# Kernel tuning notes

Hardware: AMD Instinct MI355X
Metric: run time of the kernel (lower is better)

Reference implementation:

```python
import jax, jax.numpy as jnp
import numpy as np

X_SCALE, X_ZP = 0.03, -66.0
Y_SCALE, Y_ZP = 0.025, 160.0  # per-tensor quant params for uint8 y


def setup_inputs() -> dict:
    key = jax.random.key(0)
    kx, ky = jax.random.split(key)
    # x simulates int8 values in [-128, 127], stored as fp32
    x = jax.random.randint(kx, (7, 8, 1024, 1024), 0, 256).astype(jnp.float32) - 128.0
    # y simulates uint8 values in [0, 255], stored as fp32
    y = jax.random.randint(ky, (8, 1024, 1024), 0, 256).astype(jnp.float32)
    return {"x": x, "y": y}


def reference(x, y):
    # dequantize: (q - zero_point) * scale
    qx = (x - X_ZP) * X_SCALE              # [7, B, M, K] fp32
    qy = (y - Y_ZP) * Y_SCALE              # [B, K, N] fp32
    # torch.matmul broadcasting: 4D @ 3D -> [7, B, M, N]
    return jnp.einsum('sbmk,bkn->sbmn', qx, qy)
```

## Files before the change

kernel.cpp:

```cpp
#include <hip/hip_runtime.h>
#include <cstdint>


#define NG 56

typedef int v4i  __attribute__((ext_vector_type(4)));
typedef int v16i __attribute__((ext_vector_type(16)));

#define GLOAD16(g, l) __builtin_amdgcn_global_load_lds( \
    (const __attribute__((address_space(1))) void*)(g), \
    (__attribute__((address_space(3))) void*)(l), 16, 0, 0)

__device__ __forceinline__ unsigned pack4(float4 v, float& s) {
    s += (v.x + v.y) + (v.z + v.w);
    unsigned b0 = __float_as_uint(v.x + 8388736.0f);
    unsigned b1 = __float_as_uint(v.y + 8388736.0f);
    unsigned b2 = __float_as_uint(v.z + 8388736.0f);
    unsigned b3 = __float_as_uint(v.w + 8388736.0f);
    return ((b0 & 0xFFu) | ((b1 & 0xFFu) << 8) | ((b2 & 0xFFu) << 16) | ((b3 & 0xFFu) << 24))
           ^ 0x80808080u;
}

__global__ __launch_bounds__(256) void k_prep_x(const float* __restrict__ x,
                                                unsigned char* __restrict__ xb,
                                                float* __restrict__ rx) {
    int row  = blockIdx.x * 4 + (threadIdx.x >> 6);
    int lane = threadIdx.x & 63;
    const float* src = x + (size_t)row * 1024;
    float s = 0.f;
#pragma unroll
    for (int it = 0; it < 4; ++it) {
        float4 v = *(const float4*)(src + it * 256 + lane * 4);
        unsigned p = pack4(v, s);
        *(unsigned*)&xb[(size_t)row * 1024 + it * 256 + lane * 4] = p;
    }
#pragma unroll
    for (int off = 32; off > 0; off >>= 1) s += __shfl_down(s, off);
    if (lane == 0) rx[row] = s;
}

__global__ __launch_bounds__(256) void k_prep_y(const float* __restrict__ y,
                                                unsigned char* __restrict__ yt,
                                                float* __restrict__ cy) {
    __shared__ float tile[64][65];
    __shared__ float csum[4][64];
    int b  = blockIdx.x >> 8;
    int t  = blockIdx.x & 255;
    int kt = (t >> 4) * 64, nt = (t & 15) * 64;
    int tx = threadIdx.x & 63;
    int ty = threadIdx.x >> 6;
    const float* src = y + ((size_t)b << 20) + (size_t)kt * 1024 + nt;
    float part = 0.f;
#pragma unroll
    for (int r = 0; r < 16; ++r) {
        int kk = r * 4 + ty;
        float v = src[(size_t)kk * 1024 + tx];
        tile[kk][tx] = v;
        part += v;
    }
    csum[ty][tx] = part;
    __syncthreads();
    if (threadIdx.x < 64) {
        float s = csum[0][tx] + csum[1][tx] + csum[2][tx] + csum[3][tx];
        atomicAdd(&cy[b * 1024 + nt + tx], s);
    }
    int ky = threadIdx.x & 15;
    int ny = threadIdx.x >> 4;
#pragma unroll
    for (int r = 0; r < 4; ++r) {
        int nn = r * 16 + ny;
        unsigned b0 = __float_as_uint(tile[ky * 4 + 0][nn] + 8388608.0f);
        unsigned b1 = __float_as_uint(tile[ky * 4 + 1][nn] + 8388608.0f);
        unsigned b2 = __float_as_uint(tile[ky * 4 + 2][nn] + 8388608.0f);
        unsigned b3 = __float_as_uint(tile[ky * 4 + 3][nn] + 8388608.0f);
        unsigned p = ((b0 & 0xFFu) | ((b1 & 0xFFu) << 8) | ((b2 & 0xFFu) << 16) |
                      ((b3 & 0xFFu) << 24)) ^ 0x80808080u;
        *(unsigned*)&yt[((size_t)b << 20) + (size_t)(nt + nn) * 1024 + kt + ky * 4] = p;
    }
}

__global__ __launch_bounds__(256) void k_gemm(const unsigned char* __restrict__ xb,
                                              const unsigned char* __restrict__ yt,
                                              const float* __restrict__ rx,
                                              const float* __restrict__ cy,
                                              float* __restrict__ out) {
    __shared__ __align__(16) unsigned char As[4][128 * 64];
    __shared__ __align__(16) unsigned char Bs[4][128 * 64];

    int bid = blockIdx.x;
    int wg  = (bid & 7) * (NG * 64 / 8) + (bid >> 3);
    int g   = wg >> 6;
    int t   = wg & 63;
    int m0  = (t >> 3) * 128, n0 = (t & 7) * 128;
    int b   = g & 7;

    int tid = threadIdx.x, lane = tid & 63, w = tid >> 6;
    int wm = w >> 1, wn = w & 1;

    const unsigned char* Ab = xb + (size_t)g * 1048576 + (size_t)m0 * 1024;
    const unsigned char* Bb = yt + ((size_t)b << 20) + (size_t)n0 * 1024;

    int srow   = tid >> 2;
    int schunk = (tid & 3) ^ ((srow >> 1) & 3);
    size_t off0 = (size_t)srow * 1024 + schunk * 16;
    size_t off1 = off0 + 64 * 1024;
    int dst0 = (tid & ~63) * 16;
    int dst1 = (256 + (tid & ~63)) * 16;

#define STAGE(buf, kt) do {                                   \
    GLOAD16(Ab + off0 + (size_t)(kt) * 64, &As[buf][dst0]);   \
    GLOAD16(Ab + off1 + (size_t)(kt) * 64, &As[buf][dst1]);   \
    GLOAD16(Bb + off0 + (size_t)(kt) * 64, &Bs[buf][dst0]);   \
    GLOAD16(Bb + off1 + (size_t)(kt) * 64, &Bs[buf][dst1]);   \
} while (0)

    v16i acc[2][2];
#pragma unroll
    for (int i = 0; i < 2; ++i)
#pragma unroll
        for (int j = 0; j < 2; ++j)
#pragma unroll
            for (int q = 0; q < 16; ++q) acc[i][j][q] = 0;

    int arow = lane & 31, hi = lane >> 5, key = (lane >> 1) & 3;
    int rA0 = (wm * 64 + arow) * 64, rA1 = rA0 + 32 * 64;
    int rB0 = (wn * 64 + arow) * 64, rB1 = rB0 + 32 * 64;
    int c0 = (hi ^ key) * 16;
    int c1 = ((2 + hi) ^ key) * 16;

#define COMPUTE(bi) do {                                                         \
    v4i a0k0 = *(const v4i*)&As[bi][rA0 + c0];                                   \
    v4i a1k0 = *(const v4i*)&As[bi][rA1 + c0];                                   \
    v4i b0k0 = *(const v4i*)&Bs[bi][rB0 + c0];                                   \
    v4i b1k0 = *(const v4i*)&Bs[bi][rB1 + c0];                                   \
    v4i a0k1 = *(const v4i*)&As[bi][rA0 + c1];                                   \
    v4i a1k1 = *(const v4i*)&As[bi][rA1 + c1];                                   \
    v4i b0k1 = *(const v4i*)&Bs[bi][rB0 + c1];                                   \
    v4i b1k1 = *(const v4i*)&Bs[bi][rB1 + c1];                                   \
    acc[0][0] = __builtin_amdgcn_mfma_i32_32x32x32_i8(a0k0, b0k0, acc[0][0], 0, 0, 0); \
    acc[0][1] = __builtin_amdgcn_mfma_i32_32x32x32_i8(a0k0, b1k0, acc[0][1], 0, 0, 0); \
    acc[1][0] = __builtin_amdgcn_mfma_i32_32x32x32_i8(a1k0, b0k0, acc[1][0], 0, 0, 0); \
    acc[1][1] = __builtin_amdgcn_mfma_i32_32x32x32_i8(a1k0, b1k0, acc[1][1], 0, 0, 0); \
    acc[0][0] = __builtin_amdgcn_mfma_i32_32x32x32_i8(a0k1, b0k1, acc[0][0], 0, 0, 0); \
    acc[0][1] = __builtin_amdgcn_mfma_i32_32x32x32_i8(a0k1, b1k1, acc[0][1], 0, 0, 0); \
    acc[1][0] = __builtin_amdgcn_mfma_i32_32x32x32_i8(a1k1, b0k1, acc[1][0], 0, 0, 0); \
    acc[1][1] = __builtin_amdgcn_mfma_i32_32x32x32_i8(a1k1, b1k1, acc[1][1], 0, 0, 0); \
} while (0)

    STAGE(0, 0);
    STAGE(1, 1);
    STAGE(2, 2);

    for (int kt = 0; kt < 13; ++kt) {
        asm volatile("s_waitcnt vmcnt(8)" ::: "memory");
        __syncthreads();
        STAGE((kt + 3) & 3, kt + 3);
        COMPUTE(kt & 3);
    }
    asm volatile("s_waitcnt vmcnt(8)" ::: "memory");
    __syncthreads();
    COMPUTE(1);
    asm volatile("s_waitcnt vmcnt(4)" ::: "memory");
    __syncthreads();
    COMPUTE(2);
    asm volatile("s_waitcnt vmcnt(0)" ::: "memory");
    __syncthreads();
    COMPUTE(3);
#undef COMPUTE
#undef STAGE

    const float* rxp = rx + g * 1024 + m0 + wm * 64;
    const float* cyp = cy + b * 1024 + n0 + wn * 64;
    float* og = out + (size_t)g * 1048576 + (size_t)(m0 + wm * 64) * 1024 + n0 + wn * 64;
    int col = lane & 31, r4 = hi * 4;
#pragma unroll
    for (int fi = 0; fi < 2; ++fi)
#pragma unroll
        for (int fj = 0; fj < 2; ++fj) {
            int cc = fj * 32 + col;
            float cv = cyp[cc];
            v16i v = acc[fi][fj];
#pragma unroll
            for (int q = 0; q < 16; ++q) {
                int rl = (q & 3) + 8 * (q >> 2) + r4;
                float rxv = rxp[fi * 32 + rl];
                og[(size_t)(fi * 32 + rl) * 1024 + cc] =
                    7.5e-4f * ((float)v[q] - 32.0f * rxv + 66.0f * cv - 10813440.0f);
            }
        }
}

__global__ void k_naive(const float* __restrict__ x, const float* __restrict__ y,
                        float* __restrict__ out) {
    int g = blockIdx.z, b = g & 7;
    int tx = threadIdx.x, ty = threadIdx.y;
    int m = blockIdx.y * 16 + ty, n = blockIdx.x * 16 + tx;
    __shared__ float a[16][17], bs[16][17];
    float s = 0.f;
    for (int kt = 0; kt < 64; ++kt) {
        a[ty][tx]  = x[(size_t)g * 1048576 + (size_t)m * 1024 + kt * 16 + tx];
        bs[ty][tx] = y[(size_t)b * 1048576 + (size_t)(kt * 16 + ty) * 1024 + n];
        __syncthreads();
#pragma unroll
        for (int j = 0; j < 16; ++j)
            s += ((a[ty][j] + 66.0f) * 0.03f) * ((bs[j][tx] - 160.0f) * 0.025f);
        __syncthreads();
    }
    out[(size_t)g * 1048576 + (size_t)m * 1024 + n] = s;
}

extern "C" void kernel_launch(void* const* d_in, const int* in_sizes, int n_in,
                              void* d_out, int out_size, void* d_ws, size_t ws_size,
                              hipStream_t stream) {
    const float* x = (const float*)d_in[0];
    const float* y = (const float*)d_in[1];
    float* out = (float*)d_out;

    const size_t CY_OFF = 0;
    const size_t RX_OFF = 32768;
    const size_t YT_OFF = 262144;
    const size_t XB_OFF = 262144 + 8388608ull;
    const size_t NEED   = XB_OFF + 58720256ull;

    if (ws_size >= NEED) {
        float* cy         = (float*)((char*)d_ws + CY_OFF);
        float* rx         = (float*)((char*)d_ws + RX_OFF);
        unsigned char* yt = (unsigned char*)((char*)d_ws + YT_OFF);
        unsigned char* xb = (unsigned char*)((char*)d_ws + XB_OFF);
        hipMemsetAsync(cy, 0, 32768, stream);
        k_prep_x<<<14336, 256, 0, stream>>>(x, xb, rx);
        k_prep_y<<<2048, 256, 0, stream>>>(y, yt, cy);
        k_gemm<<<NG * 64, 256, 0, stream>>>(xb, yt, rx, cy, out);
    } else {
        dim3 grid(64, 64, NG), blk(16, 16);
        k_naive<<<grid, blk, 0, stream>>>(x, y, out);
    }
}
```

Before: 226.0 us.

## Switch GEMM to 3-stage LDS pipeline with occupancy hint and explicit ds_reads

Cuts the LDS ring buffer for the int8 GEMM from four stages to three, dropping shared memory per block from 64KB to 48KB, and adds a launch-bounds hint asking for three blocks per CU. The aim is higher occupancy so memory latency is hidden across blocks rather than by deep prefetch. LDS fragment reads become inline-asm ds_read_b128 followed by a full lgkmcnt wait and a sched_barrier, and __syncthreads becomes raw s_barrier. The trade-off is less prefetch depth per block, more register pressure under the occupancy target, and a serialized read-then-MFMA schedule inside each k-step.

Result: faster. 195.3 us (-13.6%).

```diff
diff --git a/kernel.cpp b/kernel.cpp
--- a/kernel.cpp
+++ b/kernel.cpp
@@ -10,6 +10,16 @@
 #define GLOAD16(g, l) __builtin_amdgcn_global_load_lds( \
     (const __attribute__((address_space(1))) void*)(g), \
     (__attribute__((address_space(3))) void*)(l), 16, 0, 0)
+
+#define MFMA_I8(a, b, c) __builtin_amdgcn_mfma_i32_32x32x32_i8(a, b, c, 0, 0, 0)
+
+typedef __attribute__((address_space(3))) const unsigned char* lds_cptr;
+
+__device__ __forceinline__ v4i lds_read16(lds_cptr p) {
+    v4i d;
+    asm volatile("ds_read_b128 %0, %1" : "=v"(d) : "v"(p));
+    return d;
+}
 
 __device__ __forceinline__ unsigned pack4(float4 v, float& s) {
     s += (v.x + v.y) + (v.z + v.w);
@@ -79,13 +89,13 @@
     }
 }
 
-__global__ __launch_bounds__(256) void k_gemm(const unsigned char* __restrict__ xb,
-                                              const unsigned char* __restrict__ yt,
-                                              const float* __restrict__ rx,
-                                              const float* __restrict__ cy,
-                                              float* __restrict__ out) {
-    __shared__ __align__(16) unsigned char As[4][128 * 64];
-    __shared__ __align__(16) unsigned char Bs[4][128 * 64];
+__global__ __launch_bounds__(256, 3) void k_gemm(const unsigned char* __restrict__ xb,
+                                                 const unsigned char* __restrict__ yt,
+                                                 const float* __restrict__ rx,
+                                                 const float* __restrict__ cy,
+                                                 float* __restrict__ out) {
+    __shared__ __align__(16) unsigned char As[3][128 * 64];
+    __shared__ __align__(16) unsigned char Bs[3][128 * 64];
 
     int bid = blockIdx.x;
     int wg  = (bid & 7) * (NG * 64 / 8) + (bid >> 3);
@@ -129,43 +139,49 @@
     int c1 = ((2 + hi) ^ key) * 16;
 
 #define COMPUTE(bi) do {                                                         \
-    v4i a0k0 = *(const v4i*)&As[bi][rA0 + c0];                                   \
-    v4i a1k0 = *(const v4i*)&As[bi][rA1 + c0];                                   \
-    v4i b0k0 = *(const v4i*)&Bs[bi][rB0 + c0];                                   \
-    v4i b1k0 = *(const v4i*)&Bs[bi][rB1 + c0];                                   \
-    v4i a0k1 = *(const v4i*)&As[bi][rA0 + c1];                                   \
-    v4i a1k1 = *(const v4i*)&As[bi][rA1 + c1];                                   \
-    v4i b0k1 = *(const v4i*)&Bs[bi][rB0 + c1];                                   \
-    v4i b1k1 = *(const v4i*)&Bs[bi][rB1 + c1];                                   \
-    acc[0][0] = __builtin_amdgcn_mfma_i32_32x32x32_i8(a0k0, b0k0, acc[0][0], 0, 0, 0); \
-    acc[0][1] = __builtin_amdgcn_mfma_i32_32x32x32_i8(a0k0, b1k0, acc[0][1], 0, 0, 0); \
-    acc[1][0] = __builtin_amdgcn_mfma_i32_32x32x32_i8(a1k0, b0k0, acc[1][0], 0, 0, 0); \
-    acc[1][1] = __builtin_amdgcn_mfma_i32_32x32x32_i8(a1k0, b1k0, acc[1][1], 0, 0, 0); \
-    acc[0][0] = __builtin_amdgcn_mfma_i32_32x32x32_i8(a0k1, b0k1, acc[0][0], 0, 0, 0); \
-    acc[0][1] = __builtin_amdgcn_mfma_i32_32x32x32_i8(a0k1, b1k1, acc[0][1], 0, 0, 0); \
-    acc[1][0] = __builtin_amdgcn_mfma_i32_32x32x32_i8(a1k1, b0k1, acc[1][0], 0, 0, 0); \
-    acc[1][1] = __builtin_amdgcn_mfma_i32_32x32x32_i8(a1k1, b1k1, acc[1][1], 0, 0, 0); \
+    lds_cptr ap = (lds_cptr)&As[bi][0];                                          \
+    lds_cptr bp = (lds_cptr)&Bs[bi][0];                                          \
+    v4i a0k0 = lds_read16(ap + rA0 + c0);                                        \
+    v4i a1k0 = lds_read16(ap + rA1 + c0);                                        \
+    v4i b0k0 = lds_read16(bp + rB0 + c0);                                        \
+    v4i b1k0 = lds_read16(bp + rB1 + c0);                                        \
+    v4i a0k1 = lds_read16(ap + rA0 + c1);                                        \
+    v4i a1k1 = lds_read16(ap + rA1 + c1);                                        \
+    v4i b0k1 = lds_read16(bp + rB0 + c1);                                        \
+    v4i b1k1 = lds_read16(bp + rB1 + c1);                                        \
+    asm volatile("s_waitcnt lgkmcnt(0)" ::: "memory");                           \
+    __builtin_amdgcn_sched_barrier(0);                                           \
+    acc[0][0] = MFMA_I8(a0k0, b0k0, acc[0][0]);                                  \
+    acc[0][1] = MFMA_I8(a0k0, b1k0, acc[0][1]);                                  \
+    acc[1][0] = MFMA_I8(a1k0, b0k0, acc[1][0]);                                  \
+    acc[1][1] = MFMA_I8(a1k0, b1k0, acc[1][1]);                                  \
+    acc[0][0] = MFMA_I8(a0k1, b0k1, acc[0][0]);                                  \
+    acc[0][1] = MFMA_I8(a0k1, b1k1, acc[0][1]);                                  \
+    acc[1][0] = MFMA_I8(a1k1, b0k1, acc[1][0]);                                  \
+    acc[1][1] = MFMA_I8(a1k1, b1k1, acc[1][1]);                                  \
 } while (0)
 
     STAGE(0, 0);
     STAGE(1, 1);
-    STAGE(2, 2);
-
-    for (int kt = 0; kt < 13; ++kt) {
-        asm volatile("s_waitcnt vmcnt(8)" ::: "memory");
-        __syncthreads();
-        STAGE((kt + 3) & 3, kt + 3);
-        COMPUTE(kt & 3);
-    }
-    asm volatile("s_waitcnt vmcnt(8)" ::: "memory");
-    __syncthreads();
-    COMPUTE(1);
+
+    int cur = 0, nxt = 2;
+    for (int kt = 0; kt < 14; ++kt) {
+        asm volatile("s_waitcnt vmcnt(4)" ::: "memory");
+        __builtin_amdgcn_s_barrier();
+        __builtin_amdgcn_sched_barrier(0);
+        STAGE(nxt, kt + 2);
+        COMPUTE(cur);
+        cur = (cur == 2) ? 0 : cur + 1;
+        nxt = (nxt == 2) ? 0 : nxt + 1;
+    }
     asm volatile("s_waitcnt vmcnt(4)" ::: "memory");
-    __syncthreads();
+    __builtin_amdgcn_s_barrier();
+    __builtin_amdgcn_sched_barrier(0);
     COMPUTE(2);
     asm volatile("s_waitcnt vmcnt(0)" ::: "memory");
-    __syncthreads();
-    COMPUTE(3);
+    __builtin_amdgcn_s_barrier();
+    __builtin_amdgcn_sched_barrier(0);
+    COMPUTE(0);
 #undef COMPUTE
 #undef STAGE
 
```
